# Performance work log

Hardware: AMD Instinct MI355X
Metric: run time of the kernel (lower is better)

## Reference

```python
import jax, jax.numpy as jnp
import numpy as np

T, D, H, C, MAXLEN = 1024, 512, 512, 50257, 150


def setup_inputs() -> dict:
    key = jax.random.key(0)
    ks = iter(jax.random.split(key, 32))
    s = 0.1  # keep gates out of saturation
    def p(shape):
        return jax.random.normal(next(ks), shape, jnp.float32) * s
    return {
        "x": jax.random.normal(next(ks), (T, D), jnp.float32),
        "enc_Wih0": p((2, 4 * H, D)), "enc_Whh0": p((2, 4 * H, H)), "enc_b0": p((2, 4 * H)),
        "enc_Wih1": p((2, 4 * H, 2 * H)), "enc_Whh1": p((2, 4 * H, H)), "enc_b1": p((2, 4 * H)),
        "dec_Wih0": p((2, 4 * H, D)), "dec_Whh0": p((2, 4 * H, H)), "dec_b0": p((2, 4 * H)),
        "dec_Wih1": p((2, 4 * H, 2 * H)), "dec_Whh1": p((2, 4 * H, H)), "dec_b1": p((2, 4 * H)),
        "lin_W": p((C, 2 * H)), "lin_b": p((C,)),
        "emb": p((C, D)),
        "bos": p((D,)),
        "out_max_len": MAXLEN,
    }


def _cell(x, h, c, Wih, Whh, b):
    # PyTorch LSTM gate order: i, f, g, o; b = b_ih + b_hh
    g = Wih @ x + Whh @ h + b
    i, f, gg, o = jnp.split(g, 4)
    c = jax.nn.sigmoid(f) * c + jax.nn.sigmoid(i) * jnp.tanh(gg)
    h = jax.nn.sigmoid(o) * jnp.tanh(c)
    return h, c


def _run_dir(xs, Wih, Whh, b, reverse):
    Hh = Whh.shape[1]
    init = (jnp.zeros((Hh,), xs.dtype), jnp.zeros((Hh,), xs.dtype))
    def step(carry, xt):
        h, c = carry
        h, c = _cell(xt, h, c, Wih, Whh, b)
        return (h, c), h
    (hT, cT), hs = jax.lax.scan(step, init, xs, reverse=reverse)
    return hs, hT, cT  # hs aligned with input order


def _encode(x, layers):
    xs = x  # [T, D]
    h_fin, c_fin = [], []
    for (Wih, Whh, b) in layers:
        hs_f, hf, cf = _run_dir(xs, Wih[0], Whh[0], b[0], False)
        hs_b, hb, cb = _run_dir(xs, Wih[1], Whh[1], b[1], True)
        xs = jnp.concatenate([hs_f, hs_b], axis=-1)  # [T, 2H]
        h_fin.append(jnp.stack([hf, hb]))
        c_fin.append(jnp.stack([cf, cb]))
    return jnp.stack(h_fin), jnp.stack(c_fin)  # [L, 2, H]


def reference(x, enc_Wih0, enc_Whh0, enc_b0, enc_Wih1, enc_Whh1, enc_b1,
              dec_Wih0, dec_Whh0, dec_b0, dec_Wih1, dec_Whh1, dec_b1,
              lin_W, lin_b, emb, bos, out_max_len):
    layers_enc = [(enc_Wih0, enc_Whh0, enc_b0), (enc_Wih1, enc_Whh1, enc_b1)]
    layers_dec = [(dec_Wih0, dec_Whh0, dec_b0), (dec_Wih1, dec_Whh1, dec_b1)]

    h, c = _encode(x, layers_enc)  # [2, 2, H] each

    def dec_step(carry, _):
        buf, h, c = carry
        inp = buf
        nh, nc = [], []
        for l, (Wih, Whh, b) in enumerate(layers_dec):
            hf, cf = _cell(inp, h[l, 0], c[l, 0], Wih[0], Whh[0], b[0])
            hb, cb = _cell(inp, h[l, 1], c[l, 1], Wih[1], Whh[1], b[1])
            inp = jnp.concatenate([hf, hb])  # [2H]
            nh.append(jnp.stack([hf, hb]))
            nc.append(jnp.stack([cf, cb]))
        logits = lin_W @ inp + lin_b          # [C]
        tok = jnp.argmax(logits)              # greedy feedback
        buf = emb[tok]                        # [D]
        return (buf, jnp.stack(nh), jnp.stack(nc)), (logits, tok)

    _, (logits_seq, toks) = jax.lax.scan(dec_step, (bos, h, c), None, length=out_max_len)
    return logits_seq, toks  # [L_out, C], [L_out]
```

## Files before the change

### kernel.cpp

```cpp
#include <hip/hip_runtime.h>
#include <hip/hip_fp16.h>

typedef unsigned int u32;
typedef unsigned short u16;
typedef unsigned long long u64;

#define DEV static __device__ __forceinline__

DEV float sigf(float x){ return 1.0f / (1.0f + expf(-x)); }

DEV u64  ldA64(const u64* p){ return __hip_atomic_load(p, __ATOMIC_RELAXED, __HIP_MEMORY_SCOPE_AGENT); }
DEV void stA64(u64* p, u64 v){ __hip_atomic_store(p, v, __ATOMIC_RELAXED, __HIP_MEMORY_SCOPE_AGENT); }
DEV float ldAf(const float* p){ return __hip_atomic_load(p, __ATOMIC_RELAXED, __HIP_MEMORY_SCOPE_AGENT); }
DEV void stAf(float* p, float v){ __hip_atomic_store(p, v, __ATOMIC_RELAXED, __HIP_MEMORY_SCOPE_AGENT); }
DEV u32  ldA32(const u32* p){ return __hip_atomic_load(p, __ATOMIC_RELAXED, __HIP_MEMORY_SCOPE_AGENT); }

DEV u64 packHV(float h, u32 tag){ return (((u64)__float_as_uint(h)) << 32) | (u64)tag; }
DEV float unpackH(u64 v){ return __uint_as_float((u32)(v >> 32)); }

DEV u64 packKeyT(float v, u32 row, u32 tagv){
  u32 u = __float_as_uint(v);
  u = (u & 0x80000000u) ? ~u : (u | 0x80000000u);
  return (((u64)u) << 32) | ((u64)(0x1FFFFu - row) << 15) | (u64)tagv;
}

DEV float dot8h(const uint4 A, const float4 a, const float4 b){
  const __half2* h = (const __half2*)&A;
  const float2 f0 = __half22float2(h[0]);
  const float2 f1 = __half22float2(h[1]);
  const float2 f2 = __half22float2(h[2]);
  const float2 f3 = __half22float2(h[3]);
  float s;
  s  = f0.x*a.x + f0.y*a.y + f1.x*a.z + f1.y*a.w;
  s += f2.x*b.x + f2.y*b.y + f3.x*b.z + f3.y*b.w;
  return s;
}

DEV float dotrow(const float4 A, const float4 B, const float4 Cc, const float4 D,
                 const float4 q0, const float4 q1, const float4 q2, const float4 q3){
  float s;
  s  = A.x*q0.x + A.y*q0.y + A.z*q0.z + A.w*q0.w;
  s += B.x*q1.x + B.y*q1.y + B.z*q1.z + B.w*q1.w;
  s += Cc.x*q2.x + Cc.y*q2.y + Cc.z*q2.z + Cc.w*q2.w;
  s += D.x*q3.x + D.y*q3.y + D.z*q3.z + D.w*q3.w;
  return s;
}

struct SM {
  float w1s[24576];
  float inpP[1600];
  float linp[1024];
  float srow[256];
  float erow[256];
  float red[8];
  float dots[16];
  float cst0[4];
  float cst1[4];
  u64   wkey[4];
};

template<int CPT> DEV int pidx(int c){ int b = c / CPT; return b * (CPT + 4) + (c - b * CPT); }

template<int CPT, int DIN>
DEV void loadw(float* wreg, const float* Wih, const float* Whh, int jb4){
  const int tid = threadIdx.x, r = tid >> 4, p = tid & 15;
  const int R = 512 * (r >> 2) + jb4 + (r & 3);
  const float* s1 = Wih + (size_t)R * DIN;
  const float* s2 = Whh + (size_t)R * 512;
  #pragma unroll
  for (int k = 0; k < CPT; k += 4){
    const int col = p * CPT + k;
    const float4 v = *(const float4*)((col < DIN) ? (s1 + col) : (s2 + col - DIN));
    wreg[k] = v.x; wreg[k+1] = v.y; wreg[k+2] = v.z; wreg[k+3] = v.w;
  }
}

template<int CPT>
DEV void dot16(const float* wreg, const float* inpP, float* dots){
  const int tid = threadIdx.x, p = tid & 15;
  const float* xi = inpP + p * (CPT + 4);
  float acc = 0.f;
  #pragma unroll
  for (int k = 0; k < CPT; k += 4){
    const float4 xv = *(const float4*)(xi + k);
    acc = fmaf(wreg[k],   xv.x, acc);
    acc = fmaf(wreg[k+1], xv.y, acc);
    acc = fmaf(wreg[k+2], xv.z, acc);
    acc = fmaf(wreg[k+3], xv.w, acc);
  }
  #pragma unroll
  for (int s = 1; s < 16; s <<= 1) acc += __shfl_xor(acc, s, 64);
  if (p == 0) dots[tid >> 4] = acc;
}

DEV void dot16_w1(const float* w1s, const float* inpP, float* dots){
  const int tid = threadIdx.x, p = tid & 15;
  const float* xi = inpP + p * 100;
  float acc = 0.f;
  #pragma unroll
  for (int k = 0; k < 96; k += 4){
    const float4 w4 = *(const float4*)(w1s + (k >> 2) * 1024 + tid * 4);
    const float4 xv = *(const float4*)(xi + k);
    acc = fmaf(w4.x, xv.x, acc);
    acc = fmaf(w4.y, xv.y, acc);
    acc = fmaf(w4.z, xv.z, acc);
    acc = fmaf(w4.w, xv.w, acc);
  }
  #pragma unroll
  for (int s = 1; s < 16; s <<= 1) acc += __shfl_xor(acc, s, 64);
  if (p == 0) dots[tid >> 4] = acc;
}

DEV void gbar_phase(u32* g, u32 ev){
  __syncthreads();
  if (threadIdx.x == 0){
    __hip_atomic_fetch_add(g, 1u, __ATOMIC_RELEASE, __HIP_MEMORY_SCOPE_AGENT);
    const u32 tgt = 256u * ev;
    while (ldA32(g) < tgt) __builtin_amdgcn_s_sleep(8);
    (void)__hip_atomic_fetch_add(g, 0u, __ATOMIC_ACQUIRE, __HIP_MEMORY_SCOPE_AGENT);
    asm volatile("" ::: "memory");
  }
  __syncthreads();
}

template<int DIN, bool WRITE_XS>
DEV void enc_layer(const float* __restrict__ xg, float* __restrict__ xs_out,
                   const float* __restrict__ Wih, const float* __restrict__ Whh,
                   const float* __restrict__ bias,
                   u64* __restrict__ ht, float* __restrict__ hfinL, float* __restrict__ cfinL,
                   const int dir, const int jb4, SM& sm)
{
  constexpr int CPT = (DIN + 512) / 16;
  constexpr int NX  = DIN / 256;
  const int tid = threadIdx.x;
  float wreg[CPT];
  loadw<CPT, DIN>(wreg, Wih + (size_t)dir * 2048 * DIN, Whh + (size_t)dir * 2048 * 512, jb4);
  float b_i = 0.f, b_f = 0.f, b_g = 0.f, b_o = 0.f;
  if (tid < 4){
    const int j = jb4 + tid;
    sm.cst0[tid] = 0.f;
    b_i = bias[dir*2048 +        j];
    b_f = bias[dir*2048 +  512 + j];
    b_g = bias[dir*2048 + 1024 + j];
    b_o = bias[dir*2048 + 1536 + j];
  }
  float xr[NX];
  {
    const int t0 = dir ? 1023 : 0;
    #pragma unroll
    for (int i = 0; i < NX; ++i){
      const int c = tid + 256 * i;
      xr[i] = (DIN == 512) ? xg[(size_t)t0 * DIN + c] : ldAf(xg + (size_t)t0 * DIN + c);
    }
  }
  for (int step = 0; step < 1024; ++step){
    #pragma unroll
    for (int i = 0; i < NX; ++i) sm.inpP[pidx<CPT>(tid + 256 * i)] = xr[i];
    {
      const u64* hp = ht + (step & 1) * 512;
      const u32 want = (u32)step;
      u64 a = ldA64(hp + tid*2), b = ldA64(hp + tid*2 + 1);
      while ((u32)a != want){ __builtin_amdgcn_s_sleep(1); a = ldA64(hp + tid*2); }
      while ((u32)b != want){ __builtin_amdgcn_s_sleep(1); b = ldA64(hp + tid*2 + 1); }
      sm.inpP[pidx<CPT>(DIN + tid*2)]     = unpackH(a);
      sm.inpP[pidx<CPT>(DIN + tid*2 + 1)] = unpackH(b);
    }
    __syncthreads();
    if (step < 1023){
      const int tn = dir ? (1022 - step) : (step + 1);
      #pragma unroll
      for (int i = 0; i < NX; ++i){
        const int c = tid + 256 * i;
        xr[i] = (DIN == 512) ? xg[(size_t)tn * DIN + c] : ldAf(xg + (size_t)tn * DIN + c);
      }
    }
    dot16<CPT>(wreg, sm.inpP, sm.dots);
    __syncthreads();
    if (tid < 4){
      const float gi = sm.dots[tid]      + b_i;
      const float gf = sm.dots[4 + tid]  + b_f;
      const float gg = sm.dots[8 + tid]  + b_g;
      const float go = sm.dots[12 + tid] + b_o;
      const float cc = sigf(gf) * sm.cst0[tid] + sigf(gi) * tanhf(gg);
      const float hh = sigf(go) * tanhf(cc);
      sm.cst0[tid] = cc;
      const int t = dir ? (1023 - step) : step;
      const int j = jb4 + tid;
      stA64(ht + ((step + 1) & 1) * 512 + j, packHV(hh, (u32)(step + 1)));
      if (WRITE_XS) stAf(xs_out + (size_t)t * 1024 + dir * 512 + j, hh);
      if (step == 1023){ stAf(hfinL + dir*512 + j, hh); stAf(cfinL + dir*512 + j, cc); }
    }
    __syncthreads();
  }
}

__global__ void bilstm_init(u32* ws){
  for (u32 i = threadIdx.x; i < 32768u; i += 256u) ws[i] = 0u;
}

__global__ void cvt_lin(const float* __restrict__ w, uint4* __restrict__ o,
                        float* __restrict__ maxw, const int C){
  const int wv = threadIdx.x >> 6, lane = threadIdx.x & 63;
  const int stride = gridDim.x * 4;
  for (int r = blockIdx.x * 4 + wv; r < C; r += stride){
    const float4* src = (const float4*)(w + (size_t)r * 1024) + lane * 4;
    const float4 v0 = src[0], v1 = src[1], v2 = src[2], v3 = src[3];
    uint4 p0, p1;
    __half2 h;
    h = __floats2half2_rn(v0.x, v0.y); p0.x = *(const u32*)&h;
    h = __floats2half2_rn(v0.z, v0.w); p0.y = *(const u32*)&h;
    h = __floats2half2_rn(v1.x, v1.y); p0.z = *(const u32*)&h;
    h = __floats2half2_rn(v1.z, v1.w); p0.w = *(const u32*)&h;
    h = __floats2half2_rn(v2.x, v2.y); p1.x = *(const u32*)&h;
    h = __floats2half2_rn(v2.z, v2.w); p1.y = *(const u32*)&h;
    h = __floats2half2_rn(v3.x, v3.y); p1.z = *(const u32*)&h;
    h = __floats2half2_rn(v3.z, v3.w); p1.w = *(const u32*)&h;
    uint4* dst = o + (size_t)r * 128 + lane * 2;
    dst[0] = p0; dst[1] = p1;
    float m = fmaxf(fmaxf(fmaxf(fabsf(v0.x), fabsf(v0.y)), fmaxf(fabsf(v0.z), fabsf(v0.w))),
                    fmaxf(fmaxf(fabsf(v1.x), fabsf(v1.y)), fmaxf(fabsf(v1.z), fabsf(v1.w))));
    m = fmaxf(m, fmaxf(fmaxf(fabsf(v2.x), fabsf(v2.y)), fmaxf(fabsf(v2.z), fabsf(v2.w))));
    m = fmaxf(m, fmaxf(fmaxf(fabsf(v3.x), fabsf(v3.y)), fmaxf(fabsf(v3.z), fabsf(v3.w))));
    #pragma unroll
    for (int s = 1; s < 64; s <<= 1) m = fmaxf(m, __shfl_xor(m, s, 64));
    if (lane == 0) maxw[r] = m;
  }
}

template<int LINFP16>
__global__ __launch_bounds__(256, 1)
void bilstm_persist(const float* __restrict__ x,
                    const float* __restrict__ eW0, const float* __restrict__ eU0, const float* __restrict__ eb0,
                    const float* __restrict__ eW1, const float* __restrict__ eU1, const float* __restrict__ eb1,
                    const float* __restrict__ dW0, const float* __restrict__ dU0, const float* __restrict__ db0,
                    const float* __restrict__ dW1, const float* __restrict__ dU1, const float* __restrict__ db1,
                    const float* __restrict__ linW, const float* __restrict__ linb,
                    const float* __restrict__ emb, const float* __restrict__ bos,
                    float* __restrict__ out, float* __restrict__ ws, const int L, const int C)
{
  __shared__ SM sm;
  const int w = blockIdx.x;
  const int tid = threadIdx.x;
  const int dir = (w >> 2) & 1;
  const int jb4 = ((w >> 3) * 4 + (w & 3)) * 4;

  u64*  htagE = (u64*)ws;
  u64*  h0t   = htagE + 4096;
  u64*  h1t   = h0t + 2048;
  float* hfin = (float*)(h1t + 2048);
  float* cfin = hfin + 2048;
  u32*  gbar  = (u32*)(cfin + 2048);
  u64*  gkey  = (u64*)((char*)ws + 98304);
  const u16*  linH = (const u16*)((const char*)ws + 131072);
  const float* maxw = (const float*)((const char*)ws + 131072 + (size_t)C * 2048);
  float* xs1  = out;

  enc_layer<512,  true >(x,   xs1,     eW0, eU0, eb0, htagE + (0*2 + dir)*1024, hfin,        cfin,        dir, jb4, sm);
  gbar_phase(gbar, 1);
  enc_layer<1024, false>(xs1, nullptr, eW1, eU1, eb1, htagE + (1*2 + dir)*1024, hfin + 1024, cfin + 1024, dir, jb4, sm);
  gbar_phase(gbar, 2);

  float w0reg[64];
  loadw<64, 512>(w0reg, dW0 + (size_t)dir*2048*512, dU0 + (size_t)dir*2048*512, jb4);
  {
    const int r = tid >> 4, p = tid & 15;
    const int R = 512 * (r >> 2) + jb4 + (r & 3);
    const float* s1 = dW1 + (size_t)dir*2048*1024 + (size_t)R * 1024;
    const float* s2 = dU1 + (size_t)dir*2048*512  + (size_t)R * 512;
    #pragma unroll
    for (int k = 0; k < 96; k += 4){
      const int col = p * 96 + k;
      const float4 v = *(const float4*)((col < 1024) ? (s1 + col) : (s2 + col - 1024));
      *(float4*)(sm.w1s + (k >> 2) * 1024 + tid * 4) = v;
    }
  }

  float b0i=0,b0f=0,b0g=0,b0o=0, b1i=0,b1f=0,b1g=0,b1o=0;
  if (tid < 4){
    const int j = jb4 + tid;
    sm.cst0[tid] = ldAf(&cfin[dir*512 + j]);
    sm.cst1[tid] = ldAf(&cfin[1024 + dir*512 + j]);
    b0i = db0[dir*2048 + j];        b0f = db0[dir*2048 + 512 + j];
    b0g = db0[dir*2048 + 1024 + j]; b0o = db0[dir*2048 + 1536 + j];
    b1i = db1[dir*2048 + j];        b1f = db1[dir*2048 + 512 + j];
    b1g = db1[dir*2048 + 1024 + j]; b1o = db1[dir*2048 + 1536 + j];
  }
  const int rbase = w * 196 + (w < 81 ? w : 81);
  const int rn    = 196 + (w < 81 ? 1 : 0);
  int tok = 0;

  for (int t = 0; t < L; ++t){
    {
      const float* src = (t == 0) ? bos : (emb + (size_t)tok * 512);
      sm.inpP[pidx<64>(tid)]       = src[tid];
      sm.inpP[pidx<64>(tid + 256)] = src[tid + 256];
      if (t == 0){
        sm.inpP[pidx<64>(512 + tid*2)]     = ldAf(&hfin[dir*512 + tid*2]);
        sm.inpP[pidx<64>(512 + tid*2 + 1)] = ldAf(&hfin[dir*512 + tid*2 + 1]);
      } else {
        const u64* hp = h0t + (dir*2 + ((t-1) & 1)) * 512;
        const u32 want = (u32)t;
        u64 a = ldA64(hp + tid*2), b = ldA64(hp + tid*2 + 1);
        while ((u32)a != want){ __builtin_amdgcn_s_sleep(1); a = ldA64(hp + tid*2); }
        while ((u32)b != want){ __builtin_amdgcn_s_sleep(1); b = ldA64(hp + tid*2 + 1); }
        sm.inpP[pidx<64>(512 + tid*2)]     = unpackH(a);
        sm.inpP[pidx<64>(512 + tid*2 + 1)] = unpackH(b);
      }
      __syncthreads();
      dot16<64>(w0reg, sm.inpP, sm.dots);
      __syncthreads();
      if (tid < 4){
        const float gi = sm.dots[tid] + b0i, gf = sm.dots[4+tid] + b0f;
        const float gg = sm.dots[8+tid] + b0g, go = sm.dots[12+tid] + b0o;
        const float cc = sigf(gf) * sm.cst0[tid] + sigf(gi) * tanhf(gg);
        const float hh = sigf(go) * tanhf(cc);
        sm.cst0[tid] = cc;
        stA64(h0t + (dir*2 + (t & 1))*512 + jb4 + tid, packHV(hh, (u32)(t + 1)));
      }
      __syncthreads();
    }

    {
      const u32 want = (u32)(t + 1);
      #pragma unroll
      for (int i = 0; i < 4; ++i){
        const int c = tid + 256 * i;
        const int d = c >> 9, idx = c & 511;
        const u64* hp = h0t + (d*2 + (t & 1)) * 512 + idx;
        u64 v = ldA64(hp);
        while ((u32)v != want){ __builtin_amdgcn_s_sleep(1); v = ldA64(hp); }
        sm.inpP[pidx<96>(c)] = unpackH(v);
      }
      if (t == 0){
        sm.inpP[pidx<96>(1024 + tid*2)]     = ldAf(&hfin[1024 + dir*512 + tid*2]);
        sm.inpP[pidx<96>(1024 + tid*2 + 1)] = ldAf(&hfin[1024 + dir*512 + tid*2 + 1]);
      } else {
        const u64* hq = h1t + (dir*2 + ((t-1) & 1)) * 512;
        const u32 want1 = (u32)t;
        u64 e = ldA64(hq + tid*2), f = ldA64(hq + tid*2 + 1);
        while ((u32)e != want1){ __builtin_amdgcn_s_sleep(1); e = ldA64(hq + tid*2); }
        while ((u32)f != want1){ __builtin_amdgcn_s_sleep(1); f = ldA64(hq + tid*2 + 1); }
        sm.inpP[pidx<96>(1024 + tid*2)]     = unpackH(e);
        sm.inpP[pidx<96>(1024 + tid*2 + 1)] = unpackH(f);
      }
      __syncthreads();
      dot16_w1(sm.w1s, sm.inpP, sm.dots);
      __syncthreads();
      if (tid < 4){
        const float gi = sm.dots[tid] + b1i, gf = sm.dots[4+tid] + b1f;
        const float gg = sm.dots[8+tid] + b1g, go = sm.dots[12+tid] + b1o;
        const float cc = sigf(gf) * sm.cst1[tid] + sigf(gi) * tanhf(gg);
        const float hh = sigf(go) * tanhf(cc);
        sm.cst1[tid] = cc;
        stA64(h1t + (dir*2 + (t & 1))*512 + jb4 + tid, packHV(hh, (u32)(t + 1)));
      }
    }

    {
      const u32 want = (u32)(t + 1);
      float pabs = 0.f;
      #pragma unroll
      for (int i = 0; i < 4; ++i){
        const int c = tid + 256 * i;
        const int d = c >> 9, idx = c & 511;
        const u64* hp = h1t + (d*2 + (t & 1)) * 512 + idx;
        u64 v = ldA64(hp);
        while ((u32)v != want){ __builtin_amdgcn_s_sleep(1); v = ldA64(hp); }
        const float hv = unpackH(v);
        sm.linp[c] = hv;
        pabs += fabsf(hv);
      }
      const int wv = tid >> 6, lane = tid & 63;
      if constexpr (LINFP16){
        #pragma unroll
        for (int s = 1; s < 64; s <<= 1) pabs += __shfl_xor(pabs, s, 64);
        if (lane == 0) sm.red[wv] = pabs;
      }
      __syncthreads();

      const float4* ip4 = (const float4*)(sm.linp + lane * 16);
      const float4 q0 = ip4[0], q1 = ip4[1], q2 = ip4[2], q3 = ip4[3];
      u64 kmax = 0;
      const int rmaxr = rbase + rn - 1;

      if constexpr (LINFP16){
        const float sumabs = sm.red[0] + sm.red[1] + sm.red[2] + sm.red[3];
        const float cErr = sumabs * 7.5e-4f;
        float lb = -1e30f;
        for (int i0 = wv; i0 < rn; i0 += 16){
          const int ia = i0;
          const int ib = (i0 + 4  > rn - 1) ? rn - 1 : i0 + 4;
          const int ic = (i0 + 8  > rn - 1) ? rn - 1 : i0 + 8;
          const int id = (i0 + 12 > rn - 1) ? rn - 1 : i0 + 12;
          const int ra = rbase + ia, rb = rbase + ib, rc = rbase + ic, rd = rbase + id;
          const uint4* pa = (const uint4*)(linH + (size_t)ra * 1024) + lane * 2;
          const uint4* pb = (const uint4*)(linH + (size_t)rb * 1024) + lane * 2;
          const uint4* pc = (const uint4*)(linH + (size_t)rc * 1024) + lane * 2;
          const uint4* pd = (const uint4*)(linH + (size_t)rd * 1024) + lane * 2;
          const uint4 A0 = pa[0], A1 = pa[1];
          const uint4 B0 = pb[0], B1 = pb[1];
          const uint4 C0 = pc[0], C1 = pc[1];
          const uint4 D0 = pd[0], D1 = pd[1];
          float sa = dot8h(A0, q0, q1) + dot8h(A1, q2, q3);
          float sb = dot8h(B0, q0, q1) + dot8h(B1, q2, q3);
          float sc = dot8h(C0, q0, q1) + dot8h(C1, q2, q3);
          float sd = dot8h(D0, q0, q1) + dot8h(D1, q2, q3);
          #pragma unroll
          for (int sh = 1; sh < 64; sh <<= 1){
            sa += __shfl_xor(sa, sh, 64);
            sb += __shfl_xor(sb, sh, 64);
            sc += __shfl_xor(sc, sh, 64);
            sd += __shfl_xor(sd, sh, 64);
          }
          if (lane == 0){
            sa += linb[ra]; sb += linb[rb]; sc += linb[rc]; sd += linb[rd];
            out[(size_t)t * C + ra] = sa;
            out[(size_t)t * C + rb] = sb;
            out[(size_t)t * C + rc] = sc;
            out[(size_t)t * C + rd] = sd;
            const float ea = maxw[ra] * cErr + 1e-4f;
            const float eb = maxw[rb] * cErr + 1e-4f;
            const float ec = maxw[rc] * cErr + 1e-4f;
            const float ed = maxw[rd] * cErr + 1e-4f;
            sm.srow[ia] = sa; sm.erow[ia] = ea;
            sm.srow[ib] = sb; sm.erow[ib] = eb;
            sm.srow[ic] = sc; sm.erow[ic] = ec;
            sm.srow[id] = sd; sm.erow[id] = ed;
            lb = fmaxf(lb, sa - ea); lb = fmaxf(lb, sb - eb);
            lb = fmaxf(lb, sc - ec); lb = fmaxf(lb, sd - ed);
          }
        }
        if (lane == 0) sm.red[4 + wv] = lb;
        __syncthreads();
        const float Lb = fmaxf(fmaxf(sm.red[4], sm.red[5]), fmaxf(sm.red[6], sm.red[7]));
        for (int i = wv; i < rn; i += 4){
          if (sm.srow[i] + sm.erow[i] >= Lb){
            const int row = rbase + i;
            const float4* wp = (const float4*)(linW + (size_t)row * 1024) + lane * 4;
            float s = dotrow(wp[0], wp[1], wp[2], wp[3], q0, q1, q2, q3);
            #pragma unroll
            for (int sh = 1; sh < 64; sh <<= 1) s += __shfl_xor(s, sh, 64);
            if (lane == 0){
              s += linb[row];
              const u64 k = packKeyT(s, (u32)row, (u32)(t + 1));
              if (k > kmax) kmax = k;
            }
          }
        }
      } else {
        for (int i0 = wv; i0 < rn; i0 += 16){
          const int ra = rbase + i0;
          const int rb = (ra + 4  > rmaxr) ? rmaxr : ra + 4;
          const int rc = (ra + 8  > rmaxr) ? rmaxr : ra + 8;
          const int rd = (ra + 12 > rmaxr) ? rmaxr : ra + 12;
          const float ba = linb[ra], bb = linb[rb], bc = linb[rc], bd = linb[rd];
          const float4* pa = (const float4*)(linW + (size_t)ra * 1024) + lane * 4;
          const float4* pb = (const float4*)(linW + (size_t)rb * 1024) + lane * 4;
          const float4* pc = (const float4*)(linW + (size_t)rc * 1024) + lane * 4;
          const float4* pd = (const float4*)(linW + (size_t)rd * 1024) + lane * 4;
          const float4 a0 = pa[0], a1 = pa[1], a2 = pa[2], a3 = pa[3];
          const float4 e0 = pb[0], e1 = pb[1], e2 = pb[2], e3 = pb[3];
          const float4 c0 = pc[0], c1 = pc[1], c2 = pc[2], c3 = pc[3];
          const float4 d0 = pd[0], d1 = pd[1], d2 = pd[2], d3 = pd[3];
          float sa = dotrow(a0,a1,a2,a3, q0,q1,q2,q3);
          float sb = dotrow(e0,e1,e2,e3, q0,q1,q2,q3);
          float sc = dotrow(c0,c1,c2,c3, q0,q1,q2,q3);
          float sd = dotrow(d0,d1,d2,d3, q0,q1,q2,q3);
          #pragma unroll
          for (int sh = 1; sh < 64; sh <<= 1){
            sa += __shfl_xor(sa, sh, 64);
            sb += __shfl_xor(sb, sh, 64);
            sc += __shfl_xor(sc, sh, 64);
            sd += __shfl_xor(sd, sh, 64);
          }
          if (lane == 0){
            sa += ba; sb += bb; sc += bc; sd += bd;
            out[(size_t)t * C + ra] = sa;
            out[(size_t)t * C + rb] = sb;
            out[(size_t)t * C + rc] = sc;
            out[(size_t)t * C + rd] = sd;
            u64 k;
            k = packKeyT(sa, (u32)ra, (u32)(t+1)); if (k > kmax) kmax = k;
            k = packKeyT(sb, (u32)rb, (u32)(t+1)); if (k > kmax) kmax = k;
            k = packKeyT(sc, (u32)rc, (u32)(t+1)); if (k > kmax) kmax = k;
            k = packKeyT(sd, (u32)rd, (u32)(t+1)); if (k > kmax) kmax = k;
          }
        }
      }
      if (lane == 0) sm.wkey[wv] = kmax;
    }

    __syncthreads();
    if (tid == 0){
      u64 k4 = sm.wkey[0];
      if (sm.wkey[1] > k4) k4 = sm.wkey[1];
      if (sm.wkey[2] > k4) k4 = sm.wkey[2];
      if (sm.wkey[3] > k4) k4 = sm.wkey[3];
      stA64(gkey + (size_t)w * 16, k4);
    }
    __syncthreads();
    {
      const u32 wantk = (u32)(t + 1);
      const u64* p = gkey + (size_t)tid * 16;
      u64 kv = ldA64(p);
      while ((u32)(kv & 0x7FFFu) != wantk){ __builtin_amdgcn_s_sleep(1); kv = ldA64(p); }
      #pragma unroll
      for (int s = 1; s < 64; s <<= 1){
        const u64 o = (u64)__shfl_xor((unsigned long long)kv, s, 64);
        if (o > kv) kv = o;
      }
      if ((tid & 63) == 0) sm.wkey[tid >> 6] = kv;
    }
    __syncthreads();
    {
      u64 gk = sm.wkey[0];
      if (sm.wkey[1] > gk) gk = sm.wkey[1];
      if (sm.wkey[2] > gk) gk = sm.wkey[2];
      if (sm.wkey[3] > gk) gk = sm.wkey[3];
      tok = (int)(0x1FFFFu - ((u32)(gk >> 15) & 0x1FFFFu));
      if (w == 0 && tid == 0) out[(size_t)L * C + t] = (float)tok;
    }
  }
}

extern "C" void kernel_launch(void* const* d_in, const int* in_sizes, int n_in,
                              void* d_out, int out_size, void* d_ws, size_t ws_size,
                              hipStream_t stream)
{
  const float* x    = (const float*)d_in[0];
  const float* eW0  = (const float*)d_in[1];
  const float* eU0  = (const float*)d_in[2];
  const float* eb0  = (const float*)d_in[3];
  const float* eW1  = (const float*)d_in[4];
  const float* eU1  = (const float*)d_in[5];
  const float* eb1  = (const float*)d_in[6];
  const float* dW0  = (const float*)d_in[7];
  const float* dU0  = (const float*)d_in[8];
  const float* db0  = (const float*)d_in[9];
  const float* dW1  = (const float*)d_in[10];
  const float* dU1  = (const float*)d_in[11];
  const float* db1  = (const float*)d_in[12];
  const float* linW = (const float*)d_in[13];
  const float* linb = (const float*)d_in[14];
  const float* emb  = (const float*)d_in[15];
  const float* bos  = (const float*)d_in[16];

  const int C = in_sizes[14];
  const int L = out_size / (C + 1);
  const int nlin = in_sizes[13];

  const size_t need = 131072 + (size_t)nlin * 2 + (size_t)C * 4;
  const bool fp16lin = (ws_size >= need);

  hipLaunchKernelGGL(bilstm_init, dim3(1), dim3(256), 0, stream, (u32*)d_ws);
  if (fp16lin){
    hipLaunchKernelGGL(cvt_lin, dim3(2048), dim3(256), 0, stream,
                       linW, (uint4*)((char*)d_ws + 131072),
                       (float*)((char*)d_ws + 131072 + (size_t)C * 2048), C);
    hipLaunchKernelGGL((bilstm_persist<1>), dim3(256), dim3(256), 0, stream,
                       x, eW0, eU0, eb0, eW1, eU1, eb1,
                       dW0, dU0, db0, dW1, dU1, db1,
                       linW, linb, emb, bos,
                       (float*)d_out, (float*)d_ws, L, C);
  } else {
    hipLaunchKernelGGL((bilstm_persist<0>), dim3(256), dim3(256), 0, stream,
                       x, eW0, eU0, eb0, eW1, eU1, eb1,
                       dW0, dU0, db0, dW1, dU1, db1,
                       linW, linb, emb, bos,
                       (float*)d_out, (float*)d_ws, L, C);
  }
}
```

Measured before the change: 8.860 ms.

## Overlap recurrent input dots with hidden-state waits in encoder and decoder

In the encoder, the weight rows are remapped so each wavefront owns one hidden unit. The input-part dot product is computed before spinning on the previous hidden state, and the gates are evaluated with wave shuffles instead of a shared-memory round trip and an extra barrier. In the decoder, layer-1 and layer-0 hidden states are cached in shared memory rather than re-polled from global, and the layer-0 recurrent half-dot for the next step is precomputed while waiting for the global argmax. This shortens the serial per-step critical path but adds register pressure and more complex synchronisation.

```diff
diff --git a/kernel.cpp b/kernel.cpp
--- a/kernel.cpp
+++ b/kernel.cpp
@@ -50,8 +50,9 @@
   float w1s[24576];
   float inpP[1600];
   float linp[1024];
-  float srow[256];
-  float erow[256];
+  float h0c[1024];
+  float srow[200];
+  float erow[200];
   float red[8];
   float dots[16];
   float cst0[4];
@@ -75,22 +76,57 @@
   }
 }
 
-template<int CPT>
-DEV void dot16(const float* wreg, const float* inpP, float* dots){
-  const int tid = threadIdx.x, p = tid & 15;
+template<int CPT, int DIN>
+DEV void loadw_enc(float* wreg, const float* Wih, const float* Whh, int jb4){
+  const int tid = threadIdx.x, r = tid >> 4, p = tid & 15;
+  const int R = 512 * (r & 3) + jb4 + (r >> 2);
+  const float* s1 = Wih + (size_t)R * DIN;
+  const float* s2 = Whh + (size_t)R * 512;
+  #pragma unroll
+  for (int k = 0; k < CPT; k += 4){
+    const int col = p * CPT + k;
+    const float4 v = *(const float4*)((col < DIN) ? (s1 + col) : (s2 + col - DIN));
+    wreg[k] = v.x; wreg[k+1] = v.y; wreg[k+2] = v.z; wreg[k+3] = v.w;
+  }
+}
+
+template<int CPT, int DIN, bool LOW>
+DEV float dotp_reg(const float* wreg, const float* inpP, float acc){
+  const int p = threadIdx.x & 15;
   const float* xi = inpP + p * (CPT + 4);
+  #pragma unroll
+  for (int k = 0; k < CPT; k += 4){
+    const int col = p * CPT + k;
+    if ((col < DIN) == LOW){
+      const float4 xv = *(const float4*)(xi + k);
+      acc = fmaf(wreg[k],   xv.x, acc);
+      acc = fmaf(wreg[k+1], xv.y, acc);
+      acc = fmaf(wreg[k+2], xv.z, acc);
+      acc = fmaf(wreg[k+3], xv.w, acc);
+    }
+  }
+  return acc;
+}
+
+DEV void dred16(float acc, float* dots){
+  #pragma unroll
+  for (int s = 1; s < 16; s <<= 1) acc += __shfl_xor(acc, s, 64);
+  if ((threadIdx.x & 15) == 0) dots[threadIdx.x >> 4] = acc;
+}
+
+DEV float dot64_slice(const float* wreg, const float* inpP){
+  const int p = threadIdx.x & 15;
+  const float* xi = inpP + p * 68;
   float acc = 0.f;
   #pragma unroll
-  for (int k = 0; k < CPT; k += 4){
+  for (int k = 0; k < 64; k += 4){
     const float4 xv = *(const float4*)(xi + k);
     acc = fmaf(wreg[k],   xv.x, acc);
     acc = fmaf(wreg[k+1], xv.y, acc);
     acc = fmaf(wreg[k+2], xv.z, acc);
     acc = fmaf(wreg[k+3], xv.w, acc);
   }
-  #pragma unroll
-  for (int s = 1; s < 16; s <<= 1) acc += __shfl_xor(acc, s, 64);
-  if (p == 0) dots[tid >> 4] = acc;
+  return acc;
 }
 
 DEV void dot16_w1(const float* w1s, const float* inpP, float* dots){
@@ -106,9 +142,7 @@
     acc = fmaf(w4.z, xv.z, acc);
     acc = fmaf(w4.w, xv.w, acc);
   }
-  #pragma unroll
-  for (int s = 1; s < 16; s <<= 1) acc += __shfl_xor(acc, s, 64);
-  if (p == 0) dots[tid >> 4] = acc;
+  dred16(acc, dots);
 }
 
 DEV void gbar_phase(u32* g, u32 ev){
@@ -133,17 +167,15 @@
   constexpr int CPT = (DIN + 512) / 16;
   constexpr int NX  = DIN / 256;
   const int tid = threadIdx.x;
+  const int wj  = tid >> 6;
   float wreg[CPT];
-  loadw<CPT, DIN>(wreg, Wih + (size_t)dir * 2048 * DIN, Whh + (size_t)dir * 2048 * 512, jb4);
-  float b_i = 0.f, b_f = 0.f, b_g = 0.f, b_o = 0.f;
-  if (tid < 4){
-    const int j = jb4 + tid;
-    sm.cst0[tid] = 0.f;
-    b_i = bias[dir*2048 +        j];
-    b_f = bias[dir*2048 +  512 + j];
-    b_g = bias[dir*2048 + 1024 + j];
-    b_o = bias[dir*2048 + 1536 + j];
-  }
+  loadw_enc<CPT, DIN>(wreg, Wih + (size_t)dir * 2048 * DIN, Whh + (size_t)dir * 2048 * 512, jb4);
+  const int j = jb4 + wj;
+  const float b_i = bias[dir*2048 +        j];
+  const float b_f = bias[dir*2048 +  512 + j];
+  const float b_g = bias[dir*2048 + 1024 + j];
+  const float b_o = bias[dir*2048 + 1536 + j];
+  float creg = 0.f;
   float xr[NX];
   {
     const int t0 = dir ? 1023 : 0;
@@ -156,15 +188,16 @@
   for (int step = 0; step < 1024; ++step){
     #pragma unroll
     for (int i = 0; i < NX; ++i) sm.inpP[pidx<CPT>(tid + 256 * i)] = xr[i];
-    {
-      const u64* hp = ht + (step & 1) * 512;
-      const u32 want = (u32)step;
-      u64 a = ldA64(hp + tid*2), b = ldA64(hp + tid*2 + 1);
-      while ((u32)a != want){ __builtin_amdgcn_s_sleep(1); a = ldA64(hp + tid*2); }
-      while ((u32)b != want){ __builtin_amdgcn_s_sleep(1); b = ldA64(hp + tid*2 + 1); }
-      sm.inpP[pidx<CPT>(DIN + tid*2)]     = unpackH(a);
-      sm.inpP[pidx<CPT>(DIN + tid*2 + 1)] = unpackH(b);
-    }
+    __syncthreads();
+    const u64* hp = ht + (step & 1) * 512;
+    const u32 want = (u32)step;
+    u64 a = ldA64(hp + tid*2);
+    u64 b = ldA64(hp + tid*2 + 1);
+    float acc = dotp_reg<CPT, DIN, true>(wreg, sm.inpP, 0.f);
+    while ((u32)a != want){ __builtin_amdgcn_s_sleep(1); a = ldA64(hp + tid*2); }
+    while ((u32)b != want){ __builtin_amdgcn_s_sleep(1); b = ldA64(hp + tid*2 + 1); }
+    sm.inpP[pidx<CPT>(DIN + tid*2)]     = unpackH(a);
+    sm.inpP[pidx<CPT>(DIN + tid*2 + 1)] = unpackH(b);
     __syncthreads();
     if (step < 1023){
       const int tn = dir ? (1022 - step) : (step + 1);
@@ -174,23 +207,22 @@
         xr[i] = (DIN == 512) ? xg[(size_t)tn * DIN + c] : ldAf(xg + (size_t)tn * DIN + c);
       }
     }
-    dot16<CPT>(wreg, sm.inpP, sm.dots);
-    __syncthreads();
-    if (tid < 4){
-      const float gi = sm.dots[tid]      + b_i;
-      const float gf = sm.dots[4 + tid]  + b_f;
-      const float gg = sm.dots[8 + tid]  + b_g;
-      const float go = sm.dots[12 + tid] + b_o;
-      const float cc = sigf(gf) * sm.cst0[tid] + sigf(gi) * tanhf(gg);
-      const float hh = sigf(go) * tanhf(cc);
-      sm.cst0[tid] = cc;
+    acc = dotp_reg<CPT, DIN, false>(wreg, sm.inpP, acc);
+    #pragma unroll
+    for (int s = 1; s < 16; s <<= 1) acc += __shfl_xor(acc, s, 64);
+    const float gi = __shfl(acc,  0, 64) + b_i;
+    const float gf = __shfl(acc, 16, 64) + b_f;
+    const float gg = __shfl(acc, 32, 64) + b_g;
+    const float go = __shfl(acc, 48, 64) + b_o;
+    const float cc = sigf(gf) * creg + sigf(gi) * tanhf(gg);
+    const float hh = sigf(go) * tanhf(cc);
+    creg = cc;
+    if ((tid & 63) == 0){
       const int t = dir ? (1023 - step) : step;
-      const int j = jb4 + tid;
       stA64(ht + ((step + 1) & 1) * 512 + j, packHV(hh, (u32)(step + 1)));
       if (WRITE_XS) stAf(xs_out + (size_t)t * 1024 + dir * 512 + j, hh);
       if (step == 1023){ stAf(hfinL + dir*512 + j, hh); stAf(cfinL + dir*512 + j, cc); }
     }
-    __syncthreads();
   }
 }
 
@@ -288,26 +320,26 @@
   const int rbase = w * 196 + (w < 81 ? w : 81);
   const int rn    = 196 + (w < 81 ? 1 : 0);
   int tok = 0;
+  float accPre = 0.f;
 
   for (int t = 0; t < L; ++t){
+    const u32 tag = (u32)(t + 1);
     {
-      const float* src = (t == 0) ? bos : (emb + (size_t)tok * 512);
-      sm.inpP[pidx<64>(tid)]       = src[tid];
-      sm.inpP[pidx<64>(tid + 256)] = src[tid + 256];
       if (t == 0){
+        sm.inpP[pidx<64>(tid)]       = bos[tid];
+        sm.inpP[pidx<64>(tid + 256)] = bos[tid + 256];
         sm.inpP[pidx<64>(512 + tid*2)]     = ldAf(&hfin[dir*512 + tid*2]);
         sm.inpP[pidx<64>(512 + tid*2 + 1)] = ldAf(&hfin[dir*512 + tid*2 + 1]);
       } else {
-        const u64* hp = h0t + (dir*2 + ((t-1) & 1)) * 512;
-        const u32 want = (u32)t;
-        u64 a = ldA64(hp + tid*2), b = ldA64(hp + tid*2 + 1);
-        while ((u32)a != want){ __builtin_amdgcn_s_sleep(1); a = ldA64(hp + tid*2); }
-        while ((u32)b != want){ __builtin_amdgcn_s_sleep(1); b = ldA64(hp + tid*2 + 1); }
-        sm.inpP[pidx<64>(512 + tid*2)]     = unpackH(a);
-        sm.inpP[pidx<64>(512 + tid*2 + 1)] = unpackH(b);
+        const float* src = emb + (size_t)tok * 512;
+        sm.inpP[pidx<64>(tid)]       = src[tid];
+        sm.inpP[pidx<64>(tid + 256)] = src[tid + 256];
       }
       __syncthreads();
-      dot16<64>(w0reg, sm.inpP, sm.dots);
+      float acc;
+      if (t == 0) acc = dot64_slice(w0reg, sm.inpP);
+      else        acc = ((tid & 15) >= 8) ? accPre : dot64_slice(w0reg, sm.inpP);
+      dred16(acc, sm.dots);
       __syncthreads();
       if (tid < 4){
         const float gi = sm.dots[tid] + b0i, gf = sm.dots[4+tid] + b0f;
@@ -315,33 +347,29 @@
         const float cc = sigf(gf) * sm.cst0[tid] + sigf(gi) * tanhf(gg);
         const float hh = sigf(go) * tanhf(cc);
         sm.cst0[tid] = cc;
-        stA64(h0t + (dir*2 + (t & 1))*512 + jb4 + tid, packHV(hh, (u32)(t + 1)));
+        stA64(h0t + (dir*2 + (t & 1))*512 + jb4 + tid, packHV(hh, tag));
       }
       __syncthreads();
     }
 
     {
-      const u32 want = (u32)(t + 1);
       #pragma unroll
       for (int i = 0; i < 4; ++i){
         const int c = tid + 256 * i;
         const int d = c >> 9, idx = c & 511;
         const u64* hp = h0t + (d*2 + (t & 1)) * 512 + idx;
         u64 v = ldA64(hp);
-        while ((u32)v != want){ __builtin_amdgcn_s_sleep(1); v = ldA64(hp); }
-        sm.inpP[pidx<96>(c)] = unpackH(v);
+        while ((u32)v != tag){ __builtin_amdgcn_s_sleep(1); v = ldA64(hp); }
+        const float hv = unpackH(v);
+        sm.inpP[pidx<96>(c)] = hv;
+        sm.h0c[c] = hv;
       }
       if (t == 0){
         sm.inpP[pidx<96>(1024 + tid*2)]     = ldAf(&hfin[1024 + dir*512 + tid*2]);
         sm.inpP[pidx<96>(1024 + tid*2 + 1)] = ldAf(&hfin[1024 + dir*512 + tid*2 + 1]);
       } else {
-        const u64* hq = h1t + (dir*2 + ((t-1) & 1)) * 512;
-        const u32 want1 = (u32)t;
-        u64 e = ldA64(hq + tid*2), f = ldA64(hq + tid*2 + 1);
-        while ((u32)e != want1){ __builtin_amdgcn_s_sleep(1); e = ldA64(hq + tid*2); }
-        while ((u32)f != want1){ __builtin_amdgcn_s_sleep(1); f = ldA64(hq + tid*2 + 1); }
-        sm.inpP[pidx<96>(1024 + tid*2)]     = unpackH(e);
-        sm.inpP[pidx<96>(1024 + tid*2 + 1)] = unpackH(f);
+        sm.inpP[pidx<96>(1024 + tid*2)]     = sm.linp[dir*512 + tid*2];
+        sm.inpP[pidx<96>(1024 + tid*2 + 1)] = sm.linp[dir*512 + tid*2 + 1];
       }
       __syncthreads();
       dot16_w1(sm.w1s, sm.inpP, sm.dots);
@@ -352,12 +380,13 @@
         const float cc = sigf(gf) * sm.cst1[tid] + sigf(gi) * tanhf(gg);
         const float hh = sigf(go) * tanhf(cc);
         sm.cst1[tid] = cc;
-        stA64(h1t + (dir*2 + (t & 1))*512 + jb4 + tid, packHV(hh, (u32)(t + 1)));
-      }
-    }
-
+        stA64(h1t + (dir*2 + (t & 1))*512 + jb4 + tid, packHV(hh, tag));
+      }
+    }
+
+    const int wv = tid >> 6, lane = tid & 63;
+    u64 kloc;
     {
-      const u32 want = (u32)(t + 1);
       float pabs = 0.f;
       #pragma unroll
       for (int i = 0; i < 4; ++i){
@@ -365,12 +394,11 @@
         const int d = c >> 9, idx = c & 511;
         const u64* hp = h1t + (d*2 + (t & 1)) * 512 + idx;
         u64 v = ldA64(hp);
-        while ((u32)v != want){ __builtin_amdgcn_s_sleep(1); v = ldA64(hp); }
+        while ((u32)v != tag){ __builtin_amdgcn_s_sleep(1); v = ldA64(hp); }
         const float hv = unpackH(v);
         sm.linp[c] = hv;
         pabs += fabsf(hv);
       }
-      const int wv = tid >> 6, lane = tid & 63;
       if constexpr (LINFP16){
         #pragma unroll
         for (int s = 1; s < 64; s <<= 1) pabs += __shfl_xor(pabs, s, 64);
@@ -380,13 +408,13 @@
 
       const float4* ip4 = (const float4*)(sm.linp + lane * 16);
       const float4 q0 = ip4[0], q1 = ip4[1], q2 = ip4[2], q3 = ip4[3];
-      u64 kmax = 0;
+      u64 kmax = packKeyT(-3.0e38f, 0x1FFFFu, tag);
       const int rmaxr = rbase + rn - 1;
 
       if constexpr (LINFP16){
         const float sumabs = sm.red[0] + sm.red[1] + sm.red[2] + sm.red[3];
         const float cErr = sumabs * 7.5e-4f;
-        float lb = -1e30f;
+        float lb = -3.0e38f;
         for (int i0 = wv; i0 < rn; i0 += 16){
           const int ia = i0;
           const int ib = (i0 + 4  > rn - 1) ? rn - 1 : i0 + 4;
@@ -439,10 +467,10 @@
             const float4* wp = (const float4*)(linW + (size_t)row * 1024) + lane * 4;
             float s = dotrow(wp[0], wp[1], wp[2], wp[3], q0, q1, q2, q3);
             #pragma unroll
-            for (int sh = 1; sh < 64; sh <<= 1) s += __shfl_xor(s, sh, 64);
+            for (int sh2 = 1; sh2 < 64; sh2 <<= 1) s += __shfl_xor(s, sh2, 64);
             if (lane == 0){
               s += linb[row];
-              const u64 k = packKeyT(s, (u32)row, (u32)(t + 1));
+              const u64 k = packKeyT(s, (u32)row, tag);
               if (k > kmax) kmax = k;
             }
           }
@@ -458,14 +486,10 @@
           const float4* pb = (const float4*)(linW + (size_t)rb * 1024) + lane * 4;
           const float4* pc = (const float4*)(linW + (size_t)rc * 1024) + lane * 4;
           const float4* pd = (const float4*)(linW + (size_t)rd * 1024) + lane * 4;
-          const float4 a0 = pa[0], a1 = pa[1], a2 = pa[2], a3 = pa[3];
-          const float4 e0 = pb[0], e1 = pb[1], e2 = pb[2], e3 = pb[3];
-          const float4 c0 = pc[0], c1 = pc[1], c2 = pc[2], c3 = pc[3];
-          const float4 d0 = pd[0], d1 = pd[1], d2 = pd[2], d3 = pd[3];
-          float sa = dotrow(a0,a1,a2,a3, q0,q1,q2,q3);
-          float sb = dotrow(e0,e1,e2,e3, q0,q1,q2,q3);
-          float sc = dotrow(c0,c1,c2,c3, q0,q1,q2,q3);
-          float sd = dotrow(d0,d1,d2,d3, q0,q1,q2,q3);
+          float sa = dotrow(pa[0],pa[1],pa[2],pa[3], q0,q1,q2,q3);
+          float sb = dotrow(pb[0],pb[1],pb[2],pb[3], q0,q1,q2,q3);
+          float sc = dotrow(pc[0],pc[1],pc[2],pc[3], q0,q1,q2,q3);
+          float sd = dotrow(pd[0],pd[1],pd[2],pd[3], q0,q1,q2,q3);
           #pragma unroll
           for (int sh = 1; sh < 64; sh <<= 1){
             sa += __shfl_xor(sa, sh, 64);
@@ -480,16 +504,17 @@
             out[(size_t)t * C + rc] = sc;
             out[(size_t)t * C + rd] = sd;
             u64 k;
-            k = packKeyT(sa, (u32)ra, (u32)(t+1)); if (k > kmax) kmax = k;
-            k = packKeyT(sb, (u32)rb, (u32)(t+1)); if (k > kmax) kmax = k;
-            k = packKeyT(sc, (u32)rc, (u32)(t+1)); if (k > kmax) kmax = k;
-            k = packKeyT(sd, (u32)rd, (u32)(t+1)); if (k > kmax) kmax = k;
+            k = packKeyT(sa, (u32)ra, tag); if (k > kmax) kmax = k;
+            k = packKeyT(sb, (u32)rb, tag); if (k > kmax) kmax = k;
+            k = packKeyT(sc, (u32)rc, tag); if (k > kmax) kmax = k;
+            k = packKeyT(sd, (u32)rd, tag); if (k > kmax) kmax = k;
           }
         }
       }
-      if (lane == 0) sm.wkey[wv] = kmax;
-    }
-
+      kloc = kmax;
+    }
+
+    if (lane == 0) sm.wkey[wv] = kloc;
     __syncthreads();
     if (tid == 0){
       u64 k4 = sm.wkey[0];
@@ -498,12 +523,17 @@
       if (sm.wkey[3] > k4) k4 = sm.wkey[3];
       stA64(gkey + (size_t)w * 16, k4);
     }
+    if (t + 1 < L){
+      sm.inpP[pidx<64>(512 + tid*2)]     = sm.h0c[dir*512 + tid*2];
+      sm.inpP[pidx<64>(512 + tid*2 + 1)] = sm.h0c[dir*512 + tid*2 + 1];
+    }
     __syncthreads();
+    if (t + 1 < L && (tid & 15) >= 8)
+      accPre = dot64_slice(w0reg, sm.inpP);
     {
-      const u32 wantk = (u32)(t + 1);
       const u64* p = gkey + (size_t)tid * 16;
       u64 kv = ldA64(p);
-      while ((u32)(kv & 0x7FFFu) != wantk){ __builtin_amdgcn_s_sleep(1); kv = ldA64(p); }
+      while ((u32)(kv & 0x7FFFu) != tag){ __builtin_amdgcn_s_sleep(1); kv = ldA64(p); }
       #pragma unroll
       for (int s = 1; s < 64; s <<= 1){
         const u64 o = (u64)__shfl_xor((unsigned long long)kv, s, 64);
```

Measured after the change: 10.71 ms. 1.21x slower.
